# Kernel tuning notes

Measured on AMD Instinct MI355X. Metric: run time of the kernel, lower is better.

The kernel has to match this reference:

```python
import jax, jax.numpy as jnp
import numpy as np

B, F0, D = 2048, 40, 32
LAYER0, LAYER1 = 128, 128  # layer_size=(128,128), split_half=True -> field_nums=[40,64]


def setup_inputs() -> dict:
    key = jax.random.key(0)
    k1, k2, k3 = jax.random.split(key, 3)
    x = jax.random.normal(k1, (B, F0, D), dtype=jnp.float32)
    # TF conv1d filters: [1, F_prev*F0, size]; we store them reshaped [F0, F_prev_fields, size]
    # Layer 0: F_prev = F0 = 40 -> W0 flattened index m = i*F0 + j, i over x0 fields, j over hidden fields
    W0 = jax.random.normal(k2, (F0, F0, LAYER0), dtype=jnp.float32) * 0.05
    b0 = jnp.zeros((LAYER0,), dtype=jnp.float32)
    # Layer 1: F_prev = LAYER0 // 2 = 64 (split_half)
    W1 = jax.random.normal(k3, (F0, LAYER0 // 2, LAYER1), dtype=jnp.float32) * 0.05
    b1 = jnp.zeros((LAYER1,), dtype=jnp.float32)
    return {"x": x, "W0": W0, "b0": b0, "W1": W1, "b1": b1}


def reference(x, W0, b0, W1, b1):
    # CIN layer 0: outer product x0 (x) x0 over fields per embedding dim, then 1x1 conv + bias + relu
    # TF flattens dot_result as index i*F_prev + j, matching W0[i, j, s].
    h0 = jax.nn.relu(jnp.einsum('bid,bjd,ijs->bsd', x, x, W0) + b0[None, :, None])  # (B, 128, D)
    half = LAYER0 // 2
    next_hidden, direct0 = h0[:, :half, :], h0[:, half:, :]  # split_half
    # CIN layer 1 (last layer): all feature maps go to direct connect
    direct1 = jax.nn.relu(
        jnp.einsum('bid,bjd,ijs->bsd', x, next_hidden, W1) + b1[None, :, None]
    )  # (B, 128, D)
    result = jnp.concatenate([direct0, direct1], axis=1)  # (B, 192, D)
    return jnp.sum(result, axis=-1)  # (B, 192)
```

## Files before the change

### kernel.cpp

```cpp
#include <hip/hip_runtime.h>
#include <stdint.h>


typedef __attribute__((ext_vector_type(8))) _Float16 half8;
typedef __attribute__((ext_vector_type(2))) _Float16 half2v;
typedef __attribute__((ext_vector_type(4))) float f32x4;

#define T0 30
#define T1P 81
#define PERIOD 3
#define WBUF 12288

__host__ __device__ constexpr int ic0_of(int t) {
    return (t < 2) ? t : (t < 6) ? (t - 2) : (t < 12) ? (t - 6)
         : (t < 20) ? (t - 12) : (t - 20);
}
__host__ __device__ constexpr int jc0_of(int t) {
    return (t < 2) ? 0 : (t < 6) ? 1 : (t < 12) ? 2 : (t < 20) ? 3 : 4;
}

__device__ __forceinline__ unsigned short f2h(float f) {
    return __builtin_bit_cast(unsigned short, (_Float16)f);
}
__device__ __forceinline__ float qsum(float v) {
    v += __shfl_xor(v, 16, 64);
    v += __shfl_xor(v, 32, 64);
    return v;
}
__device__ __forceinline__ void gl_lds16(const unsigned short* g, unsigned short* l) {
    __builtin_amdgcn_global_load_lds(
        (const __attribute__((address_space(1))) unsigned int*)g,
        (__attribute__((address_space(3))) unsigned int*)l,
        16, 0, 0);
}

__global__ void permute_w_both(const float* __restrict__ W0, const float* __restrict__ W1,
                               unsigned short* __restrict__ Wp0, unsigned short* __restrict__ Wp1)
{
    const int t = blockIdx.x;
    const int tid = threadIdx.x;
    unsigned short outv[16];
    unsigned short* dst;
    if (t < T0) {
        const int ic = ic0_of(t), jc = jc0_of(t);
        #pragma unroll
        for (int q = 0; q < 16; ++q) {
            int pos  = tid * 16 + q;
            int oc   = pos & 7, lane = (pos >> 3) & 63;
            int nt   = (pos >> 9) & 3, sh = pos >> 11;
            int s    = sh * 64 + nt * 16 + (lane & 15);
            int i    = ic * 4 + (lane >> 4), j = jc * 8 + oc;
            float v = 0.0f;
            if (i < j)       v = W0[((size_t)(i * 40 + j)) * 128 + s]
                               + W0[((size_t)(j * 40 + i)) * 128 + s];
            else if (i == j) v = W0[((size_t)(i * 40 + i)) * 128 + s];
            outv[q] = f2h(v);
        }
        dst = Wp0 + (size_t)t * 4096 + tid * 16;
    } else {
        const int tt = t - T0;
        if (tt == 80) {
            #pragma unroll
            for (int q = 0; q < 16; ++q) outv[q] = 0;
        } else {
            const int jc = tt / 10, ic = tt % 10;
            #pragma unroll
            for (int q = 0; q < 16; ++q) {
                int pos  = tid * 16 + q;
                int oc   = pos & 7, lane = (pos >> 3) & 63;
                int nt   = (pos >> 9) & 3, sh = pos >> 11;
                int s    = sh * 64 + nt * 16 + (lane & 15);
                int i    = ic * 4 + (lane >> 4), j = jc * 8 + oc;
                outv[q] = f2h(W1[((size_t)(i * 64 + j)) * 128 + s]);
            }
        }
        dst = Wp1 + (size_t)tt * 4096 + tid * 16;
    }
    *(uint4*)dst       = *(const uint4*)outv;
    *(uint4*)(dst + 8) = *(const uint4*)(outv + 8);
}

template<int T, int PHASE>
__device__ __forceinline__ void gemm_phase(
    const unsigned short* __restrict__ Wp,
    const unsigned short* __restrict__ Jl,
    int jstride,
    const unsigned int xi_pk[2][10],
    unsigned short* Wb,
    f32x4 acc[4][2], int tid)
{
    const int lane = tid & 63;
    const int wv = tid >> 6;
    const int rt = wv >> 2;
    const int sq = wv & 3;
    const int ml = lane & 15;

    const unsigned short* jbase = Jl + (rt * 64 + ml) * jstride;

    const unsigned short* brd = Wb + (sq >> 1) * 2048 + (sq & 1) * 1024 + lane * 8;
    const unsigned short* gsrc = Wp + tid * 8;
    unsigned short* ldstA = Wb + wv * 512;
    unsigned short* ldstB = Wb + 8192 + wv * 512;

    auto stage_period = [&](int buf, int t0) {
        gl_lds16(gsrc + (size_t)t0 * 4096, ldstA + buf * WBUF);
        if (wv < 8)
            gl_lds16(gsrc + (size_t)(t0 + 2) * 4096, ldstB + buf * WBUF);
    };

    stage_period(0, 0);
    __syncthreads();

    uint4 jv[4];
    constexpr int NP = T / PERIOD;
    #pragma unroll
    for (int p = 0; p < NP; ++p) {
        const int cb = p & 1;
        const int nb = cb ^ 1;
        if ((p + 1) * PERIOD < T) stage_period(nb, (p + 1) * PERIOD);
        #pragma unroll
        for (int u = 0; u < PERIOD; ++u) {
            const int t  = p * PERIOD + u;
            const int ic = (PHASE == 0) ? ic0_of(t) : (t % 10);
            const int jc = (PHASE == 0) ? jc0_of(t) : (t / 10);
            const bool rl = (t == 0) ||
                (jc != ((PHASE == 0) ? jc0_of(t - 1) : ((t - 1) / 10)));
            if (rl) {
                #pragma unroll
                for (int mt = 0; mt < 4; ++mt)
                    jv[mt] = *(const uint4*)(jbase + mt * 16 * jstride + jc * 8);
            }
            uint4 av[4];
            #pragma unroll
            for (int pr = 0; pr < 2; ++pr) {
                half2v xp = __builtin_bit_cast(half2v, xi_pk[pr][ic]);
                half2v x0 = {xp[0], xp[0]};
                half2v x1 = {xp[1], xp[1]};
                av[2*pr].x   = __builtin_bit_cast(unsigned int, (half2v)(x0 * __builtin_bit_cast(half2v, jv[2*pr].x)));
                av[2*pr].y   = __builtin_bit_cast(unsigned int, (half2v)(x0 * __builtin_bit_cast(half2v, jv[2*pr].y)));
                av[2*pr].z   = __builtin_bit_cast(unsigned int, (half2v)(x0 * __builtin_bit_cast(half2v, jv[2*pr].z)));
                av[2*pr].w   = __builtin_bit_cast(unsigned int, (half2v)(x0 * __builtin_bit_cast(half2v, jv[2*pr].w)));
                av[2*pr+1].x = __builtin_bit_cast(unsigned int, (half2v)(x1 * __builtin_bit_cast(half2v, jv[2*pr+1].x)));
                av[2*pr+1].y = __builtin_bit_cast(unsigned int, (half2v)(x1 * __builtin_bit_cast(half2v, jv[2*pr+1].y)));
                av[2*pr+1].z = __builtin_bit_cast(unsigned int, (half2v)(x1 * __builtin_bit_cast(half2v, jv[2*pr+1].z)));
                av[2*pr+1].w = __builtin_bit_cast(unsigned int, (half2v)(x1 * __builtin_bit_cast(half2v, jv[2*pr+1].w)));
            }
            #pragma unroll
            for (int nt = 0; nt < 2; ++nt) {
                uint4 bv = *(const uint4*)(brd + cb * WBUF + u * 4096 + nt * 512);
                #pragma unroll
                for (int mt = 0; mt < 4; ++mt)
                    acc[mt][nt] = __builtin_amdgcn_mfma_f32_16x16x32_f16(
                        __builtin_bit_cast(half8, av[mt]),
                        __builtin_bit_cast(half8, bv), acc[mt][nt], 0, 0, 0);
            }
        }
        __syncthreads();
    }
}

__global__ __launch_bounds__(1024, 4)
void fused_two_layer(const float* __restrict__ x,
                     const unsigned short* __restrict__ W0p,
                     const float* __restrict__ b0,
                     const unsigned short* __restrict__ W1p,
                     const float* __restrict__ b1,
                     float* __restrict__ out)
{
    __shared__ __align__(16) unsigned short Xl[256 * 40];
    __shared__ __align__(16) unsigned short NH[256 * 72];
    __shared__ __align__(16) unsigned short Wb[2 * WBUF];

    const int tid  = threadIdx.x;
    const int lane = tid & 63;
    const int wv   = tid >> 6;
    const int rt   = wv >> 2;
    const int sq   = wv & 3;
    const int ml   = lane & 15;
    const int kc   = lane >> 4;

    const float* xblk = x + (size_t)blockIdx.x * (8 * 40 * 32);
    #pragma unroll
    for (int k = 0; k < 10; ++k) {
        int f = 1024 * k + tid;
        int bl = f / 1280, rem = f - bl * 1280;
        int i = rem >> 5, d = rem & 31;
        Xl[(bl * 32 + d) * 40 + i] = f2h(xblk[f]);
    }
    __syncthreads();

    unsigned int xi_pk[2][10];
    #pragma unroll
    for (int pr = 0; pr < 2; ++pr) {
        const unsigned short* xr0 = Xl + (rt * 64 + pr * 32 + ml) * 40;
        const unsigned short* xr1 = xr0 + 16 * 40;
        #pragma unroll
        for (int ic = 0; ic < 10; ++ic) {
            unsigned int u0 = xr0[ic * 4 + kc];
            unsigned int u1 = xr1[ic * 4 + kc];
            xi_pk[pr][ic] = u0 | (u1 << 16);
        }
    }

    f32x4 acc[4][2];
    const f32x4 zero4 = {0.f, 0.f, 0.f, 0.f};
    #pragma unroll
    for (int mt = 0; mt < 4; ++mt)
        #pragma unroll
        for (int nt = 0; nt < 2; ++nt) acc[mt][nt] = zero4;

    gemm_phase<T0, 0>(W0p, Xl, 40, xi_pk, Wb, acc, tid);

    {
        float bias[2];
        #pragma unroll
        for (int nt = 0; nt < 2; ++nt) bias[nt] = b0[sq * 32 + nt * 16 + ml];
        if (sq < 2) {
            #pragma unroll
            for (int mt = 0; mt < 4; ++mt) {
                int r = rt * 64 + mt * 16 + (kc << 2);
                #pragma unroll
                for (int nt = 0; nt < 2; ++nt) {
                    int s = sq * 32 + nt * 16 + ml;
                    #pragma unroll
                    for (int rg = 0; rg < 4; ++rg) {
                        float v = fmaxf(acc[mt][nt][rg] + bias[nt], 0.0f);
                        NH[(r + rg) * 72 + s] = f2h(v);
                    }
                }
            }
        } else {
            int bb = blockIdx.x * 8 + rt * 2;
            #pragma unroll
            for (int nt = 0; nt < 2; ++nt) {
                float sA = 0.f, sB = 0.f;
                #pragma unroll
                for (int rg = 0; rg < 4; ++rg) {
                    sA += fmaxf(acc[0][nt][rg] + bias[nt], 0.f)
                        + fmaxf(acc[1][nt][rg] + bias[nt], 0.f);
                    sB += fmaxf(acc[2][nt][rg] + bias[nt], 0.f)
                        + fmaxf(acc[3][nt][rg] + bias[nt], 0.f);
                }
                sA = qsum(sA); sB = qsum(sB);
                if (lane < 16) {
                    int col = (sq - 2) * 32 + nt * 16 + lane;
                    out[(size_t)bb * 192 + col]       = sA;
                    out[(size_t)(bb + 1) * 192 + col] = sB;
                }
            }
            if (sq == 2) {
                int a = (rt * 64 + lane) * 72 + 64;
                *(uint2*)&NH[a]     = (uint2){0u, 0u};
                *(uint2*)&NH[a + 4] = (uint2){0u, 0u};
            }
        }
    }
    __syncthreads();

    #pragma unroll
    for (int mt = 0; mt < 4; ++mt)
        #pragma unroll
        for (int nt = 0; nt < 2; ++nt) acc[mt][nt] = zero4;

    gemm_phase<T1P, 1>(W1p, NH, 72, xi_pk, Wb, acc, tid);

    {
        float bias[2];
        #pragma unroll
        for (int nt = 0; nt < 2; ++nt) bias[nt] = b1[sq * 32 + nt * 16 + ml];
        int bb = blockIdx.x * 8 + rt * 2;
        #pragma unroll
        for (int nt = 0; nt < 2; ++nt) {
            float sA = 0.f, sB = 0.f;
            #pragma unroll
            for (int rg = 0; rg < 4; ++rg) {
                sA += fmaxf(acc[0][nt][rg] + bias[nt], 0.f)
                    + fmaxf(acc[1][nt][rg] + bias[nt], 0.f);
                sB += fmaxf(acc[2][nt][rg] + bias[nt], 0.f)
                    + fmaxf(acc[3][nt][rg] + bias[nt], 0.f);
            }
            sA = qsum(sA); sB = qsum(sB);
            if (lane < 16) {
                int col = 64 + sq * 32 + nt * 16 + lane;
                out[(size_t)bb * 192 + col]       = sA;
                out[(size_t)(bb + 1) * 192 + col] = sB;
            }
        }
    }
}

extern "C" void kernel_launch(void* const* d_in, const int* in_sizes, int n_in,
                              void* d_out, int out_size, void* d_ws, size_t ws_size,
                              hipStream_t stream) {
    const float* x  = (const float*)d_in[0];
    const float* W0 = (const float*)d_in[1];
    const float* b0 = (const float*)d_in[2];
    const float* W1 = (const float*)d_in[3];
    const float* b1 = (const float*)d_in[4];
    float* out = (float*)d_out;

    unsigned short* W0p = (unsigned short*)d_ws;
    unsigned short* W1p = (unsigned short*)((char*)d_ws + T0 * 4096 * 2);

    permute_w_both<<<T0 + T1P, 256, 0, stream>>>(W0, W1, W0p, W1p);
    fused_two_layer<<<256, 1024, 0, stream>>>(x, W0p, b0, W1p, b1, out);
}
```

Before: 120.9 us.

## Switch CIN GEMMs from 16x16x32 to 32x32x16 MFMA tiles

Replaces the 4x2 grid of 16x16x32 f16 MFMAs per wave with two 32x32x16 MFMAs per k-half. The weight permutation layout, x-field packing, A-operand construction and epilogue row mapping change to match the new operand and accumulator layouts. This cuts MFMA instruction count and A-side LDS reads and elementwise multiplies per step. In exchange it changes the reduction pattern in the epilogue, and the larger instruction's latency may need enough independent accumulators to hide.

```diff
diff --git a/kernel.cpp b/kernel.cpp
--- a/kernel.cpp
+++ b/kernel.cpp
@@ -4,7 +4,7 @@
 
 typedef __attribute__((ext_vector_type(8))) _Float16 half8;
 typedef __attribute__((ext_vector_type(2))) _Float16 half2v;
-typedef __attribute__((ext_vector_type(4))) float f32x4;
+typedef __attribute__((ext_vector_type(16))) float f32x16;
 
 #define T0 30
 #define T1P 81
@@ -21,17 +21,20 @@
 
 __device__ __forceinline__ unsigned short f2h(float f) {
     return __builtin_bit_cast(unsigned short, (_Float16)f);
-}
-__device__ __forceinline__ float qsum(float v) {
-    v += __shfl_xor(v, 16, 64);
-    v += __shfl_xor(v, 32, 64);
-    return v;
 }
 __device__ __forceinline__ void gl_lds16(const unsigned short* g, unsigned short* l) {
     __builtin_amdgcn_global_load_lds(
         (const __attribute__((address_space(1))) unsigned int*)g,
         (__attribute__((address_space(3))) unsigned int*)l,
         16, 0, 0);
+}
+__device__ __forceinline__ uint4 avmul(half2v xs, uint4 jv) {
+    uint4 r;
+    r.x = __builtin_bit_cast(unsigned int, (half2v)(xs * __builtin_bit_cast(half2v, jv.x)));
+    r.y = __builtin_bit_cast(unsigned int, (half2v)(xs * __builtin_bit_cast(half2v, jv.y)));
+    r.z = __builtin_bit_cast(unsigned int, (half2v)(xs * __builtin_bit_cast(half2v, jv.z)));
+    r.w = __builtin_bit_cast(unsigned int, (half2v)(xs * __builtin_bit_cast(half2v, jv.w)));
+    return r;
 }
 
 __global__ void permute_w_both(const float* __restrict__ W0, const float* __restrict__ W1,
@@ -46,10 +49,11 @@
         #pragma unroll
         for (int q = 0; q < 16; ++q) {
             int pos  = tid * 16 + q;
-            int oc   = pos & 7, lane = (pos >> 3) & 63;
-            int nt   = (pos >> 9) & 3, sh = pos >> 11;
-            int s    = sh * 64 + nt * 16 + (lane & 15);
-            int i    = ic * 4 + (lane >> 4), j = jc * 8 + oc;
+            int e    = pos & 7, lane = (pos >> 3) & 63;
+            int kh   = (pos >> 9) & 1, sq = pos >> 10;
+            int s    = sq * 32 + (lane & 31);
+            int i    = ic * 4 + kh * 2 + (lane >> 5);
+            int j    = jc * 8 + e;
             float v = 0.0f;
             if (i < j)       v = W0[((size_t)(i * 40 + j)) * 128 + s]
                                + W0[((size_t)(j * 40 + i)) * 128 + s];
@@ -67,10 +71,11 @@
             #pragma unroll
             for (int q = 0; q < 16; ++q) {
                 int pos  = tid * 16 + q;
-                int oc   = pos & 7, lane = (pos >> 3) & 63;
-                int nt   = (pos >> 9) & 3, sh = pos >> 11;
-                int s    = sh * 64 + nt * 16 + (lane & 15);
-                int i    = ic * 4 + (lane >> 4), j = jc * 8 + oc;
+                int e    = pos & 7, lane = (pos >> 3) & 63;
+                int kh   = (pos >> 9) & 1, sq = pos >> 10;
+                int s    = sq * 32 + (lane & 31);
+                int i    = ic * 4 + kh * 2 + (lane >> 5);
+                int j    = jc * 8 + e;
                 outv[q] = f2h(W1[((size_t)(i * 64 + j)) * 128 + s]);
             }
         }
@@ -85,19 +90,19 @@
     const unsigned short* __restrict__ Wp,
     const unsigned short* __restrict__ Jl,
     int jstride,
-    const unsigned int xi_pk[2][10],
+    const unsigned int xk[2][10],
     unsigned short* Wb,
-    f32x4 acc[4][2], int tid)
+    f32x16 acc[2], int tid)
 {
     const int lane = tid & 63;
     const int wv = tid >> 6;
     const int rt = wv >> 2;
     const int sq = wv & 3;
-    const int ml = lane & 15;
-
-    const unsigned short* jbase = Jl + (rt * 64 + ml) * jstride;
-
-    const unsigned short* brd = Wb + (sq >> 1) * 2048 + (sq & 1) * 1024 + lane * 8;
+    const int c31 = lane & 31;
+
+    const unsigned short* jbase = Jl + (rt * 64 + c31) * jstride;
+
+    const unsigned short* brd = Wb + sq * 1024 + lane * 8;
     const unsigned short* gsrc = Wp + tid * 8;
     unsigned short* ldstA = Wb + wv * 512;
     unsigned short* ldstB = Wb + 8192 + wv * 512;
@@ -111,7 +116,7 @@
     stage_period(0, 0);
     __syncthreads();
 
-    uint4 jv[4];
+    uint4 jv0, jv1;
     constexpr int NP = T / PERIOD;
     #pragma unroll
     for (int p = 0; p < NP; ++p) {
@@ -126,33 +131,22 @@
             const bool rl = (t == 0) ||
                 (jc != ((PHASE == 0) ? jc0_of(t - 1) : ((t - 1) / 10)));
             if (rl) {
-                #pragma unroll
-                for (int mt = 0; mt < 4; ++mt)
-                    jv[mt] = *(const uint4*)(jbase + mt * 16 * jstride + jc * 8);
-            }
-            uint4 av[4];
-            #pragma unroll
-            for (int pr = 0; pr < 2; ++pr) {
-                half2v xp = __builtin_bit_cast(half2v, xi_pk[pr][ic]);
+                jv0 = *(const uint4*)(jbase + jc * 8);
+                jv1 = *(const uint4*)(jbase + 32 * jstride + jc * 8);
+            }
+            const unsigned short* bb_ = brd + cb * WBUF + u * 4096;
+            #pragma unroll
+            for (int kh = 0; kh < 2; ++kh) {
+                uint4 bvv = *(const uint4*)(bb_ + kh * 512);
+                half2v xp = __builtin_bit_cast(half2v, xk[kh][ic]);
                 half2v x0 = {xp[0], xp[0]};
                 half2v x1 = {xp[1], xp[1]};
-                av[2*pr].x   = __builtin_bit_cast(unsigned int, (half2v)(x0 * __builtin_bit_cast(half2v, jv[2*pr].x)));
-                av[2*pr].y   = __builtin_bit_cast(unsigned int, (half2v)(x0 * __builtin_bit_cast(half2v, jv[2*pr].y)));
-                av[2*pr].z   = __builtin_bit_cast(unsigned int, (half2v)(x0 * __builtin_bit_cast(half2v, jv[2*pr].z)));
-                av[2*pr].w   = __builtin_bit_cast(unsigned int, (half2v)(x0 * __builtin_bit_cast(half2v, jv[2*pr].w)));
-                av[2*pr+1].x = __builtin_bit_cast(unsigned int, (half2v)(x1 * __builtin_bit_cast(half2v, jv[2*pr+1].x)));
-                av[2*pr+1].y = __builtin_bit_cast(unsigned int, (half2v)(x1 * __builtin_bit_cast(half2v, jv[2*pr+1].y)));
-                av[2*pr+1].z = __builtin_bit_cast(unsigned int, (half2v)(x1 * __builtin_bit_cast(half2v, jv[2*pr+1].z)));
-                av[2*pr+1].w = __builtin_bit_cast(unsigned int, (half2v)(x1 * __builtin_bit_cast(half2v, jv[2*pr+1].w)));
-            }
-            #pragma unroll
-            for (int nt = 0; nt < 2; ++nt) {
-                uint4 bv = *(const uint4*)(brd + cb * WBUF + u * 4096 + nt * 512);
-                #pragma unroll
-                for (int mt = 0; mt < 4; ++mt)
-                    acc[mt][nt] = __builtin_amdgcn_mfma_f32_16x16x32_f16(
-                        __builtin_bit_cast(half8, av[mt]),
-                        __builtin_bit_cast(half8, bv), acc[mt][nt], 0, 0, 0);
+                acc[0] = __builtin_amdgcn_mfma_f32_32x32x16_f16(
+                    __builtin_bit_cast(half8, avmul(x0, jv0)),
+                    __builtin_bit_cast(half8, bvv), acc[0], 0, 0, 0);
+                acc[1] = __builtin_amdgcn_mfma_f32_32x32x16_f16(
+                    __builtin_bit_cast(half8, avmul(x1, jv1)),
+                    __builtin_bit_cast(half8, bvv), acc[1], 0, 0, 0);
             }
         }
         __syncthreads();
@@ -176,8 +170,8 @@
     const int wv   = tid >> 6;
     const int rt   = wv >> 2;
     const int sq   = wv & 3;
-    const int ml   = lane & 15;
-    const int kc   = lane >> 4;
+    const int c31  = lane & 31;
+    const int hb   = lane >> 5;
 
     const float* xblk = x + (size_t)blockIdx.x * (8 * 40 * 32);
     #pragma unroll
@@ -189,102 +183,78 @@
     }
     __syncthreads();
 
-    unsigned int xi_pk[2][10];
-    #pragma unroll
-    for (int pr = 0; pr < 2; ++pr) {
-        const unsigned short* xr0 = Xl + (rt * 64 + pr * 32 + ml) * 40;
-        const unsigned short* xr1 = xr0 + 16 * 40;
-        #pragma unroll
-        for (int ic = 0; ic < 10; ++ic) {
-            unsigned int u0 = xr0[ic * 4 + kc];
-            unsigned int u1 = xr1[ic * 4 + kc];
-            xi_pk[pr][ic] = u0 | (u1 << 16);
-        }
-    }
-
-    f32x4 acc[4][2];
-    const f32x4 zero4 = {0.f, 0.f, 0.f, 0.f};
-    #pragma unroll
-    for (int mt = 0; mt < 4; ++mt)
-        #pragma unroll
-        for (int nt = 0; nt < 2; ++nt) acc[mt][nt] = zero4;
-
-    gemm_phase<T0, 0>(W0p, Xl, 40, xi_pk, Wb, acc, tid);
-
+    unsigned int xk[2][10];
     {
-        float bias[2];
-        #pragma unroll
-        for (int nt = 0; nt < 2; ++nt) bias[nt] = b0[sq * 32 + nt * 16 + ml];
+        const unsigned short* xr0 = Xl + (rt * 64 + c31) * 40;
+        const unsigned short* xr1 = xr0 + 32 * 40;
+        #pragma unroll
+        for (int ic = 0; ic < 10; ++ic)
+            #pragma unroll
+            for (int kh = 0; kh < 2; ++kh) {
+                unsigned int u0 = xr0[ic * 4 + kh * 2 + hb];
+                unsigned int u1 = xr1[ic * 4 + kh * 2 + hb];
+                xk[kh][ic] = u0 | (u1 << 16);
+            }
+    }
+
+    f32x16 acc[2];
+    #pragma unroll
+    for (int rtt = 0; rtt < 2; ++rtt)
+        #pragma unroll
+        for (int rg = 0; rg < 16; ++rg) acc[rtt][rg] = 0.f;
+
+    gemm_phase<T0, 0>(W0p, Xl, 40, xk, Wb, acc, tid);
+
+    {
+        float bs = b0[sq * 32 + c31];
         if (sq < 2) {
             #pragma unroll
-            for (int mt = 0; mt < 4; ++mt) {
-                int r = rt * 64 + mt * 16 + (kc << 2);
+            for (int rtt = 0; rtt < 2; ++rtt)
                 #pragma unroll
-                for (int nt = 0; nt < 2; ++nt) {
-                    int s = sq * 32 + nt * 16 + ml;
-                    #pragma unroll
-                    for (int rg = 0; rg < 4; ++rg) {
-                        float v = fmaxf(acc[mt][nt][rg] + bias[nt], 0.0f);
-                        NH[(r + rg) * 72 + s] = f2h(v);
-                    }
+                for (int rg = 0; rg < 16; ++rg) {
+                    int row = rt * 64 + rtt * 32 + (rg & 3) + 8 * (rg >> 2) + 4 * hb;
+                    NH[row * 72 + sq * 32 + c31] =
+                        f2h(fmaxf(acc[rtt][rg] + bs, 0.0f));
                 }
-            }
         } else {
-            int bb = blockIdx.x * 8 + rt * 2;
-            #pragma unroll
-            for (int nt = 0; nt < 2; ++nt) {
-                float sA = 0.f, sB = 0.f;
+            #pragma unroll
+            for (int rtt = 0; rtt < 2; ++rtt) {
+                float s = 0.f;
                 #pragma unroll
-                for (int rg = 0; rg < 4; ++rg) {
-                    sA += fmaxf(acc[0][nt][rg] + bias[nt], 0.f)
-                        + fmaxf(acc[1][nt][rg] + bias[nt], 0.f);
-                    sB += fmaxf(acc[2][nt][rg] + bias[nt], 0.f)
-                        + fmaxf(acc[3][nt][rg] + bias[nt], 0.f);
-                }
-                sA = qsum(sA); sB = qsum(sB);
-                if (lane < 16) {
-                    int col = (sq - 2) * 32 + nt * 16 + lane;
-                    out[(size_t)bb * 192 + col]       = sA;
-                    out[(size_t)(bb + 1) * 192 + col] = sB;
-                }
+                for (int rg = 0; rg < 16; ++rg)
+                    s += fmaxf(acc[rtt][rg] + bs, 0.0f);
+                s += __shfl_xor(s, 32, 64);
+                int bb = blockIdx.x * 8 + rt * 2 + rtt;
+                if (lane < 32)
+                    out[(size_t)bb * 192 + (sq - 2) * 32 + c31] = s;
             }
             if (sq == 2) {
                 int a = (rt * 64 + lane) * 72 + 64;
-                *(uint2*)&NH[a]     = (uint2){0u, 0u};
-                *(uint2*)&NH[a + 4] = (uint2){0u, 0u};
+                *(uint4*)&NH[a] = (uint4){0u, 0u, 0u, 0u};
             }
         }
     }
     __syncthreads();
 
     #pragma unroll
-    for (int mt = 0; mt < 4; ++mt)
-        #pragma unroll
-        for (int nt = 0; nt < 2; ++nt) acc[mt][nt] = zero4;
-
-    gemm_phase<T1P, 1>(W1p, NH, 72, xi_pk, Wb, acc, tid);
+    for (int rtt = 0; rtt < 2; ++rtt)
+        #pragma unroll
+        for (int rg = 0; rg < 16; ++rg) acc[rtt][rg] = 0.f;
+
+    gemm_phase<T1P, 1>(W1p, NH, 72, xk, Wb, acc, tid);
 
     {
-        float bias[2];
-        #pragma unroll
-        for (int nt = 0; nt < 2; ++nt) bias[nt] = b1[sq * 32 + nt * 16 + ml];
-        int bb = blockIdx.x * 8 + rt * 2;
-        #pragma unroll
-        for (int nt = 0; nt < 2; ++nt) {
-            float sA = 0.f, sB = 0.f;
-            #pragma unroll
-            for (int rg = 0; rg < 4; ++rg) {
-                sA += fmaxf(acc[0][nt][rg] + bias[nt], 0.f)
-                    + fmaxf(acc[1][nt][rg] + bias[nt], 0.f);
-                sB += fmaxf(acc[2][nt][rg] + bias[nt], 0.f)
-                    + fmaxf(acc[3][nt][rg] + bias[nt], 0.f);
-            }
-            sA = qsum(sA); sB = qsum(sB);
-            if (lane < 16) {
-                int col = 64 + sq * 32 + nt * 16 + lane;
-                out[(size_t)bb * 192 + col]       = sA;
-                out[(size_t)(bb + 1) * 192 + col] = sB;
-            }
+        float bs = b1[sq * 32 + c31];
+        #pragma unroll
+        for (int rtt = 0; rtt < 2; ++rtt) {
+            float s = 0.f;
+            #pragma unroll
+            for (int rg = 0; rg < 16; ++rg)
+                s += fmaxf(acc[rtt][rg] + bs, 0.0f);
+            s += __shfl_xor(s, 32, 64);
+            int bb = blockIdx.x * 8 + rt * 2 + rtt;
+            if (lane < 32)
+                out[(size_t)bb * 192 + 64 + sq * 32 + c31] = s;
         }
     }
 }
```

After: 121.6 us. Within noise of the previous version (+0.5%).
